# Kernel tuning notes

Measured on AMD Instinct MI355X. Metric: run time of the kernel, lower is better.

Reference implementation:

```python
import jax, jax.numpy as jnp
import numpy as np

N = 512          # number of proposals
C = 1024         # in_channels
FLAT = C * 7 * 7 # 50176, fc1 input dim
D = 1024         # hidden / feat_dim / attention dim
SCALE = 1.0 / np.sqrt(float(D))


def setup_inputs() -> dict:
    key = jax.random.key(0)
    ks = jax.random.split(key, 20)
    w = lambda k, shape: (jax.random.normal(k, shape, jnp.float32) * 0.01)
    inp = {"x": jax.random.normal(ks[0], (N, C, 7, 7), jnp.float32)}
    # SelsaHead fc layers
    inp["fc1_w"] = w(ks[1], (D, FLAT)); inp["fc1_b"] = jnp.zeros((D,), jnp.float32)
    inp["fc2_w"] = w(ks[2], (D, D));    inp["fc2_b"] = jnp.zeros((D,), jnp.float32)
    # attention_1 (semantic_aggregation): fc1, fc2, 1x1 conv (stored as [D,D] matrix)
    inp["a1_fc1_w"] = w(ks[3], (D, D)); inp["a1_fc1_b"] = jnp.zeros((D,), jnp.float32)
    inp["a1_fc2_w"] = w(ks[4], (D, D)); inp["a1_fc2_b"] = jnp.zeros((D,), jnp.float32)
    inp["a1_conv_w"] = w(ks[5], (D, D)); inp["a1_conv_b"] = jnp.zeros((D,), jnp.float32)
    # attention_2
    inp["a2_fc1_w"] = w(ks[6], (D, D)); inp["a2_fc1_b"] = jnp.zeros((D,), jnp.float32)
    inp["a2_fc2_w"] = w(ks[7], (D, D)); inp["a2_fc2_b"] = jnp.zeros((D,), jnp.float32)
    inp["a2_conv_w"] = w(ks[8], (D, D)); inp["a2_conv_b"] = jnp.zeros((D,), jnp.float32)
    return inp


def _semantic_aggregation(x, w1, b1, w2, b2, cw, cb):
    # x: [N, D]. Single-head dense attention over proposals, values = x itself.
    q = x @ w1.T + b1                      # [N, D]
    k = x @ w2.T + b2                      # [N, D]
    p = jax.nn.softmax((q @ k.T) * SCALE, axis=-1)  # [N, N]
    out = p @ x                            # [N, D]  (values are raw x)
    return out @ cw.T + cb                 # 1x1 conv == linear [N, D]


def reference(x, fc1_w, fc1_b, fc2_w, fc2_b,
              a1_fc1_w, a1_fc1_b, a1_fc2_w, a1_fc2_b, a1_conv_w, a1_conv_b,
              a2_fc1_w, a2_fc1_b, a2_fc2_w, a2_fc2_b, a2_conv_w, a2_conv_b):
    out = x.reshape(x.shape[0], -1) @ fc1_w.T + fc1_b        # [N, D]
    r1 = _semantic_aggregation(out, a1_fc1_w, a1_fc1_b, a1_fc2_w, a1_fc2_b,
                               a1_conv_w, a1_conv_b)
    h = jax.nn.relu(out + r1)
    h = h @ fc2_w.T + fc2_b                                  # [N, D]
    r2 = _semantic_aggregation(h, a2_fc1_w, a2_fc1_b, a2_fc2_w, a2_fc2_b,
                               a2_conv_w, a2_conv_b)
    return jax.nn.relu(h + r2 + out)                         # [N, D]
```

## Files before the change

### kernel.cpp

```cpp
#include <hip/hip_runtime.h>
#include <hip/hip_bf16.h>

typedef __attribute__((ext_vector_type(8))) short short8;
typedef __attribute__((ext_vector_type(4))) float f32x4;

#define N_PROP 512
#define DHID   1024
#define KFLAT  50176
#define SM_SCALE 0.03125f

__device__ inline short f2bf(float x) {
  __hip_bfloat16 b = __float2bfloat16(x);
  return __builtin_bit_cast(short, b);
}
__device__ inline float bf2f(unsigned short u) {
  unsigned int x = (unsigned int)u << 16;
  return __builtin_bit_cast(float, x);
}

__global__ __launch_bounds__(1024, 4)
void gemm_fc1(const float* __restrict__ A, const float* __restrict__ B,
              __hip_bfloat16* __restrict__ parts)
{
  constexpr int BK = 32, BKP = 40;
  constexpr int KLEN = 1568, NT = KLEN / BK;
  __shared__ short sA[2][256 * BKP];
  __shared__ short sB[2][256 * BKP];

  const int n = gridDim.x;
  int lid = blockIdx.x;
  lid = (lid & 7) * (n >> 3) + (lid >> 3);
  const int y    = lid >> 3;
  const int tile = lid & 7;
  const int tm = tile >> 2;
  const int tn = tile & 3;

  const int k0 = y * KLEN;

  const int tid  = threadIdx.x;
  const int lane = tid & 63;
  const int wid  = tid >> 6;
  const int wr = wid >> 2, wc = wid & 3;
  const int l16 = lane & 15, kq = lane >> 4;

  const float* Ab = A + (size_t)(tm * 256) * KFLAT;
  const float* Bb = B + (size_t)(tn * 256) * KFLAT;

  const int srow = tid >> 2;
  const int scol = (tid & 3) * 8;

  f32x4 acc[4][4];
  #pragma unroll
  for (int i = 0; i < 4; ++i)
    #pragma unroll
    for (int j = 0; j < 4; ++j)
      acc[i][j] = (f32x4){0.f, 0.f, 0.f, 0.f};

  float4 ra0, ra1, rb0, rb1;

  auto loadAB = [&](int kk) {
    const float* pa = Ab + (size_t)srow * KFLAT + kk + scol;
    const float* pb = Bb + (size_t)srow * KFLAT + kk + scol;
    ra0 = *(const float4*)pa; ra1 = *(const float4*)(pa + 4);
    rb0 = *(const float4*)pb; rb1 = *(const float4*)(pb + 4);
  };
  auto storeAB = [&](int b) {
    short8 s;
    s[0]=f2bf(ra0.x); s[1]=f2bf(ra0.y); s[2]=f2bf(ra0.z); s[3]=f2bf(ra0.w);
    s[4]=f2bf(ra1.x); s[5]=f2bf(ra1.y); s[6]=f2bf(ra1.z); s[7]=f2bf(ra1.w);
    *(short8*)&sA[b][srow * BKP + scol] = s;
    s[0]=f2bf(rb0.x); s[1]=f2bf(rb0.y); s[2]=f2bf(rb0.z); s[3]=f2bf(rb0.w);
    s[4]=f2bf(rb1.x); s[5]=f2bf(rb1.y); s[6]=f2bf(rb1.z); s[7]=f2bf(rb1.w);
    *(short8*)&sB[b][srow * BKP + scol] = s;
  };
  auto compute = [&](int b) {
    short8 af[4], bf[4];
    #pragma unroll
    for (int i = 0; i < 4; ++i)
      af[i] = *(short8*)&sA[b][(wr * 64 + i * 16 + l16) * BKP + kq * 8];
    #pragma unroll
    for (int j = 0; j < 4; ++j)
      bf[j] = *(short8*)&sB[b][(wc * 64 + j * 16 + l16) * BKP + kq * 8];
    #pragma unroll
    for (int i = 0; i < 4; ++i)
      #pragma unroll
      for (int j = 0; j < 4; ++j)
        acc[i][j] = __builtin_amdgcn_mfma_f32_16x16x32_bf16(af[i], bf[j], acc[i][j], 0, 0, 0);
  };

  loadAB(k0);
  storeAB(0);
  loadAB(k0 + BK);
  __syncthreads();

  int cur = 0;
  for (int t = 0; t < NT; ++t) {
    if (t + 1 < NT) {
      storeAB(cur ^ 1);
      if (t + 2 < NT) loadAB(k0 + (t + 2) * BK);
    }
    compute(cur);
    __syncthreads();
    cur ^= 1;
  }

  __hip_bfloat16* P = parts + (size_t)y * (N_PROP * DHID);
  const int crow0 = tm * 256 + wr * 64;
  const int ccol0 = tn * 256 + wc * 64;
  #pragma unroll
  for (int i = 0; i < 4; ++i)
    #pragma unroll
    for (int j = 0; j < 4; ++j)
      #pragma unroll
      for (int e = 0; e < 4; ++e) {
        int r = crow0 + i * 16 + kq * 4 + e;
        int c = ccol0 + j * 16 + l16;
        P[(size_t)r * DHID + c] = __float2bfloat16(acc[i][j][e]);
      }
}

template<int BM, int BN, int BK, int MINW>
__global__ __launch_bounds__(256, MINW)
void gemm_nt(const float* __restrict__ A, int lda,
             const float* __restrict__ B1, const float* __restrict__ B2, int ldb,
             float* __restrict__ C, __hip_bfloat16* __restrict__ Cb, int ldc,
             int tiles_per_slice, int tiles_n,
             int klen, int ktot,
             size_t c_split_stride, size_t c_z_stride,
             const float* __restrict__ bias1, const float* __restrict__ bias2,
             const float* __restrict__ res1, const float* __restrict__ res2,
             float* __restrict__ Ct, int ldct,
             int do_relu)
{
  constexpr int BKP = BK + 8;
  constexpr int WM = BM / 2, WN = BN / 2;
  constexpr int FM = WM / 16, FN = WN / 16;
  constexpr int NCH = BK / 8;
  constexpr int CHA = (BM * BK) / (8 * 256);
  constexpr int CHB = (BN * BK) / (8 * 256);

  __shared__ short As[BM * BKP];
  __shared__ short Bs[BN * BKP];

  const int n = gridDim.x;
  int lid = blockIdx.x;
  lid = (lid & 7) * (n >> 3) + (lid >> 3);

  const int y    = lid / tiles_per_slice;
  const int tile = lid % tiles_per_slice;
  const int tm = tile / tiles_n;
  const int tn = tile % tiles_n;

  const int k0 = y * klen;
  const int krem = ktot - k0;
  const int klen_eff = krem < klen ? krem : klen;
  const int nt = klen_eff / BK;

  const size_t coff = (size_t)y * c_split_stride + (size_t)blockIdx.z * c_z_stride;
  if (C)  C  += coff;
  if (Cb) Cb += coff;
  const float* B    = blockIdx.z ? B2 : B1;
  const float* bias = blockIdx.z ? bias2 : bias1;

  const int tid  = threadIdx.x;
  const int lane = tid & 63;
  const int wid  = tid >> 6;
  const int wm = wid >> 1, wn = wid & 1;
  const int l16 = lane & 15, kq = lane >> 4;

  const float* Abase = A + (size_t)(tm * BM) * lda;
  const float* Bbase = B + (size_t)(tn * BN) * ldb;

  f32x4 acc[FM][FN];
  #pragma unroll
  for (int i = 0; i < FM; ++i)
    #pragma unroll
    for (int j = 0; j < FN; ++j)
      acc[i][j] = (f32x4){0.f, 0.f, 0.f, 0.f};

  float4 ra[CHA][2], rb[CHB][2];

  auto loadA = [&](int kk) {
    #pragma unroll
    for (int i = 0; i < CHA; ++i) {
      int ch = tid + i * 256;
      int r = ch / NCH, cc = ch % NCH;
      const float* p = Abase + (size_t)r * lda + kk + cc * 8;
      ra[i][0] = *(const float4*)p;
      ra[i][1] = *(const float4*)(p + 4);
    }
  };
  auto loadB = [&](int kk) {
    #pragma unroll
    for (int i = 0; i < CHB; ++i) {
      int ch = tid + i * 256;
      int r = ch / NCH, cc = ch % NCH;
      const float* p = Bbase + (size_t)r * ldb + kk + cc * 8;
      rb[i][0] = *(const float4*)p;
      rb[i][1] = *(const float4*)(p + 4);
    }
  };
  auto storeAB = [&]() {
    #pragma unroll
    for (int i = 0; i < CHA; ++i) {
      int ch = tid + i * 256;
      int r = ch / NCH, cc = ch % NCH;
      float4 u = ra[i][0], v = ra[i][1];
      short8 s;
      s[0]=f2bf(u.x); s[1]=f2bf(u.y); s[2]=f2bf(u.z); s[3]=f2bf(u.w);
      s[4]=f2bf(v.x); s[5]=f2bf(v.y); s[6]=f2bf(v.z); s[7]=f2bf(v.w);
      *(short8*)&As[r * BKP + cc * 8] = s;
    }
    #pragma unroll
    for (int i = 0; i < CHB; ++i) {
      int ch = tid + i * 256;
      int r = ch / NCH, cc = ch % NCH;
      float4 u = rb[i][0], v = rb[i][1];
      short8 s;
      s[0]=f2bf(u.x); s[1]=f2bf(u.y); s[2]=f2bf(u.z); s[3]=f2bf(u.w);
      s[4]=f2bf(v.x); s[5]=f2bf(v.y); s[6]=f2bf(v.z); s[7]=f2bf(v.w);
      *(short8*)&Bs[r * BKP + cc * 8] = s;
    }
  };

  loadA(k0); loadB(k0);
  storeAB();
  __syncthreads();

  for (int t = 0; t < nt; ++t) {
    if (t + 1 < nt) { loadA(k0 + (t + 1) * BK); loadB(k0 + (t + 1) * BK); }

    #pragma unroll
    for (int ks = 0; ks < BK / 32; ++ks) {
      short8 af[FM], bf[FN];
      #pragma unroll
      for (int i = 0; i < FM; ++i)
        af[i] = *(short8*)&As[(wm * WM + i * 16 + l16) * BKP + ks * 32 + kq * 8];
      #pragma unroll
      for (int j = 0; j < FN; ++j)
        bf[j] = *(short8*)&Bs[(wn * WN + j * 16 + l16) * BKP + ks * 32 + kq * 8];
      #pragma unroll
      for (int i = 0; i < FM; ++i)
        #pragma unroll
        for (int j = 0; j < FN; ++j)
          acc[i][j] = __builtin_amdgcn_mfma_f32_16x16x32_bf16(af[i], bf[j], acc[i][j], 0, 0, 0);
    }

    __syncthreads();
    if (t + 1 < nt) storeAB();
    __syncthreads();
  }

  const int crow0 = tm * BM + wm * WM;
  const int ccol0 = tn * BN + wn * WN;
  #pragma unroll
  for (int i = 0; i < FM; ++i)
    #pragma unroll
    for (int j = 0; j < FN; ++j)
      #pragma unroll
      for (int e = 0; e < 4; ++e) {
        int r = crow0 + i * 16 + kq * 4 + e;
        int c = ccol0 + j * 16 + l16;
        float v = acc[i][j][e];
        if (bias) v += bias[c];
        if (res1) v += res1[(size_t)r * ldc + c];
        if (res2) v += res2[(size_t)r * ldc + c];
        if (do_relu) v = fmaxf(v, 0.f);
        if (Cb) Cb[(size_t)r * ldc + c] = __float2bfloat16(v);
        else    C [(size_t)r * ldc + c] = v;
        if (Ct) Ct[(size_t)c * ldct + r] = v;
      }
}

__global__ __launch_bounds__(256)
void reduce_bias(const __hip_bfloat16* __restrict__ parts, int sk, size_t stride,
                 const float* __restrict__ bias, float* __restrict__ out)
{
  int idx4 = blockIdx.x * 256 + threadIdx.x;
  int c4 = idx4 & (DHID / 4 - 1);
  float4 b = *(const float4*)(bias + (size_t)c4 * 4);
  float s0 = b.x, s1 = b.y, s2 = b.z, s3 = b.w;
  for (int i = 0; i < sk; ++i) {
    const __hip_bfloat16* p = parts + (size_t)i * stride + (size_t)idx4 * 4;
    ushort4 u = *(const ushort4*)p;
    s0 += bf2f(u.x); s1 += bf2f(u.y); s2 += bf2f(u.z); s3 += bf2f(u.w);
  }
  float4 o = {s0, s1, s2, s3};
  *(float4*)(out + (size_t)idx4 * 4) = o;
}

__global__ __launch_bounds__(256)
void transpose_k(const float* __restrict__ in, float* __restrict__ out, int R, int Cc)
{
  __shared__ float t[32][33];
  int bx = blockIdx.x * 32;
  int by = blockIdx.y * 32;
  int tx = threadIdx.x & 31, ty = threadIdx.x >> 5;
  #pragma unroll
  for (int i = 0; i < 4; ++i)
    t[ty + i * 8][tx] = in[(size_t)(by + ty + i * 8) * Cc + bx + tx];
  __syncthreads();
  #pragma unroll
  for (int i = 0; i < 4; ++i)
    out[(size_t)(bx + ty + i * 8) * R + by + tx] = t[tx][ty + i * 8];
}

__global__ __launch_bounds__(256)
void softmax_rows(float* __restrict__ x, float scale)
{
  int row = blockIdx.x;
  float* p = x + (size_t)row * N_PROP;
  int tid = threadIdx.x;
  float a = p[tid] * scale;
  float b = p[tid + 256] * scale;
  float m = fmaxf(a, b);
  #pragma unroll
  for (int o = 32; o > 0; o >>= 1) m = fmaxf(m, __shfl_xor(m, o));
  __shared__ float sm[4], ss[4];
  int w = tid >> 6;
  if ((tid & 63) == 0) sm[w] = m;
  __syncthreads();
  m = fmaxf(fmaxf(sm[0], sm[1]), fmaxf(sm[2], sm[3]));
  float ea = __expf(a - m), eb = __expf(b - m);
  float s = ea + eb;
  #pragma unroll
  for (int o = 32; o > 0; o >>= 1) s += __shfl_xor(s, o);
  if ((tid & 63) == 0) ss[w] = s;
  __syncthreads();
  s = ss[0] + ss[1] + ss[2] + ss[3];
  float inv = 1.f / s;
  p[tid] = ea * inv;
  p[tid + 256] = eb * inv;
}

extern "C" void kernel_launch(void* const* d_in, const int* in_sizes, int n_in,
                              void* d_out, int out_size, void* d_ws, size_t ws_size,
                              hipStream_t stream)
{
  (void)in_sizes; (void)n_in; (void)out_size; (void)ws_size;
  const float* x      = (const float*)d_in[0];
  const float* fc1_w  = (const float*)d_in[1];
  const float* fc1_b  = (const float*)d_in[2];
  const float* fc2_w  = (const float*)d_in[3];
  const float* fc2_b  = (const float*)d_in[4];
  const float* a1w1   = (const float*)d_in[5];
  const float* a1b1   = (const float*)d_in[6];
  const float* a1w2   = (const float*)d_in[7];
  const float* a1b2   = (const float*)d_in[8];
  const float* a1cw   = (const float*)d_in[9];
  const float* a1cb   = (const float*)d_in[10];
  const float* a2w1   = (const float*)d_in[11];
  const float* a2b1   = (const float*)d_in[12];
  const float* a2w2   = (const float*)d_in[13];
  const float* a2b2   = (const float*)d_in[14];
  const float* a2cw   = (const float*)d_in[15];
  const float* a2cb   = (const float*)d_in[16];
  float* out = (float*)d_out;

  char* ws = (char*)d_ws;
  const size_t SZ = (size_t)N_PROP * DHID * 4;
  float* out0   = (float*)(ws + 0 * SZ);
  float* h0     = (float*)(ws + 1 * SZ);
  float* h1     = (float*)(ws + 2 * SZ);
  float* T      = (float*)(ws + 3 * SZ);
  float* q      = (float*)(ws + 4 * SZ);
  float* k      = (float*)(ws + 5 * SZ);
  float* att    = (float*)(ws + 6 * SZ);
  float* logits = (float*)(ws + 7 * SZ);
  __hip_bfloat16* parts =
      (__hip_bfloat16*)(ws + 7 * SZ + (size_t)N_PROP * N_PROP * 4);

  const size_t ND = (size_t)N_PROP * DHID;
  const int SK = 32;
  dim3 blk(256);

  gemm_fc1<<<dim3(8 * SK), dim3(1024), 0, stream>>>(x, fc1_w, parts);
  reduce_bias<<<(N_PROP * DHID) / 1024, blk, 0, stream>>>(parts, SK, ND, fc1_b, out0);

  transpose_k<<<dim3(DHID / 32, N_PROP / 32), blk, 0, stream>>>(out0, T, N_PROP, DHID);
  gemm_nt<32, 64, 128, 2><<<dim3(256, 1, 2), blk, 0, stream>>>(
      out0, DHID, a1w1, a1w2, DHID,
      q, nullptr, DHID,
      256, 16, DHID, DHID,
      0, ND,
      a1b1, a1b2, nullptr, nullptr, nullptr, 0, 0);
  gemm_nt<32, 32, 128, 2><<<dim3(256), blk, 0, stream>>>(
      q, DHID, k, nullptr, DHID,
      logits, nullptr, N_PROP,
      256, 16, DHID, DHID,
      0, 0,
      nullptr, nullptr, nullptr, nullptr, nullptr, 0, 0);
  softmax_rows<<<N_PROP, blk, 0, stream>>>(logits, SM_SCALE);
  gemm_nt<32, 64, 128, 2><<<dim3(256), blk, 0, stream>>>(
      logits, N_PROP, T, nullptr, N_PROP,
      att, nullptr, DHID,
      256, 16, N_PROP, N_PROP,
      0, 0,
      nullptr, nullptr, nullptr, nullptr, nullptr, 0, 0);
  gemm_nt<32, 64, 128, 2><<<dim3(256), blk, 0, stream>>>(
      att, DHID, a1cw, nullptr, DHID,
      h0, nullptr, DHID,
      256, 16, DHID, DHID,
      0, 0,
      a1cb, nullptr, out0, nullptr, nullptr, 0, 1);
  gemm_nt<32, 64, 128, 2><<<dim3(256), blk, 0, stream>>>(
      h0, DHID, fc2_w, nullptr, DHID,
      h1, nullptr, DHID,
      256, 16, DHID, DHID,
      0, 0,
      fc2_b, nullptr, nullptr, nullptr, T, N_PROP, 0);

  gemm_nt<32, 64, 128, 2><<<dim3(256, 1, 2), blk, 0, stream>>>(
      h1, DHID, a2w1, a2w2, DHID,
      q, nullptr, DHID,
      256, 16, DHID, DHID,
      0, ND,
      a2b1, a2b2, nullptr, nullptr, nullptr, 0, 0);
  gemm_nt<32, 32, 128, 2><<<dim3(256), blk, 0, stream>>>(
      q, DHID, k, nullptr, DHID,
      logits, nullptr, N_PROP,
      256, 16, DHID, DHID,
      0, 0,
      nullptr, nullptr, nullptr, nullptr, nullptr, 0, 0);
  softmax_rows<<<N_PROP, blk, 0, stream>>>(logits, SM_SCALE);
  gemm_nt<32, 64, 128, 2><<<dim3(256), blk, 0, stream>>>(
      logits, N_PROP, T, nullptr, N_PROP,
      att, nullptr, DHID,
      256, 16, N_PROP, N_PROP,
      0, 0,
      nullptr, nullptr, nullptr, nullptr, nullptr, 0, 0);
  gemm_nt<32, 64, 128, 2><<<dim3(256), blk, 0, stream>>>(
      att, DHID, a2cw, nullptr, DHID,
      out, nullptr, DHID,
      256, 16, DHID, DHID,
      0, 0,
      a2cb, nullptr, h1, out0, nullptr, 0, 1);
}
```

Before: 218.0 us.

## Swizzle fc1 LDS tiles with XOR layout and use lightweight LDS-only barriers

Replaces the padded LDS rows (stride 40) in the fc1 GEMM with an unpadded 32-element row and an XOR swizzle of the 8-element chunk index, to avoid bank conflicts while shrinking LDS use. It also replaces __syncthreads with a barrier that waits only on LDS counters, so outstanding global prefetch loads are not drained at each barrier. The swizzled layout must match between writes and reads, and the weaker barrier relies on global loads not being needed before the sync.

```diff
diff --git a/kernel.cpp b/kernel.cpp
--- a/kernel.cpp
+++ b/kernel.cpp
@@ -18,14 +18,20 @@
   return __builtin_bit_cast(float, x);
 }
 
+__device__ inline void pinned_bar() {
+  asm volatile("s_waitcnt lgkmcnt(0)" ::: "memory");
+  __builtin_amdgcn_s_barrier();
+  asm volatile("" ::: "memory");
+}
+
 __global__ __launch_bounds__(1024, 4)
 void gemm_fc1(const float* __restrict__ A, const float* __restrict__ B,
               __hip_bfloat16* __restrict__ parts)
 {
-  constexpr int BK = 32, BKP = 40;
+  constexpr int BK = 32;
   constexpr int KLEN = 1568, NT = KLEN / BK;
-  __shared__ short sA[2][256 * BKP];
-  __shared__ short sB[2][256 * BKP];
+  __shared__ short sA[2][256 * 32];
+  __shared__ short sB[2][256 * 32];
 
   const int n = gridDim.x;
   int lid = blockIdx.x;
@@ -47,7 +53,8 @@
   const float* Bb = B + (size_t)(tn * 256) * KFLAT;
 
   const int srow = tid >> 2;
-  const int scol = (tid & 3) * 8;
+  const int sc   = tid & 3;
+  const int sphys = sc ^ ((srow >> 1) & 3);
 
   f32x4 acc[4][4];
   #pragma unroll
@@ -59,8 +66,8 @@
   float4 ra0, ra1, rb0, rb1;
 
   auto loadAB = [&](int kk) {
-    const float* pa = Ab + (size_t)srow * KFLAT + kk + scol;
-    const float* pb = Bb + (size_t)srow * KFLAT + kk + scol;
+    const float* pa = Ab + (size_t)srow * KFLAT + kk + sc * 8;
+    const float* pb = Bb + (size_t)srow * KFLAT + kk + sc * 8;
     ra0 = *(const float4*)pa; ra1 = *(const float4*)(pa + 4);
     rb0 = *(const float4*)pb; rb1 = *(const float4*)(pb + 4);
   };
@@ -68,19 +75,25 @@
     short8 s;
     s[0]=f2bf(ra0.x); s[1]=f2bf(ra0.y); s[2]=f2bf(ra0.z); s[3]=f2bf(ra0.w);
     s[4]=f2bf(ra1.x); s[5]=f2bf(ra1.y); s[6]=f2bf(ra1.z); s[7]=f2bf(ra1.w);
-    *(short8*)&sA[b][srow * BKP + scol] = s;
+    *(short8*)&sA[b][srow * 32 + sphys * 8] = s;
     s[0]=f2bf(rb0.x); s[1]=f2bf(rb0.y); s[2]=f2bf(rb0.z); s[3]=f2bf(rb0.w);
     s[4]=f2bf(rb1.x); s[5]=f2bf(rb1.y); s[6]=f2bf(rb1.z); s[7]=f2bf(rb1.w);
-    *(short8*)&sB[b][srow * BKP + scol] = s;
+    *(short8*)&sB[b][srow * 32 + sphys * 8] = s;
   };
   auto compute = [&](int b) {
     short8 af[4], bf[4];
     #pragma unroll
-    for (int i = 0; i < 4; ++i)
-      af[i] = *(short8*)&sA[b][(wr * 64 + i * 16 + l16) * BKP + kq * 8];
-    #pragma unroll
-    for (int j = 0; j < 4; ++j)
-      bf[j] = *(short8*)&sB[b][(wc * 64 + j * 16 + l16) * BKP + kq * 8];
+    for (int i = 0; i < 4; ++i) {
+      int R  = wr * 64 + i * 16 + l16;
+      int ph = kq ^ ((R >> 1) & 3);
+      af[i] = *(short8*)&sA[b][R * 32 + ph * 8];
+    }
+    #pragma unroll
+    for (int j = 0; j < 4; ++j) {
+      int R  = wc * 64 + j * 16 + l16;
+      int ph = kq ^ ((R >> 1) & 3);
+      bf[j] = *(short8*)&sB[b][R * 32 + ph * 8];
+    }
     #pragma unroll
     for (int i = 0; i < 4; ++i)
       #pragma unroll
@@ -91,7 +104,7 @@
   loadAB(k0);
   storeAB(0);
   loadAB(k0 + BK);
-  __syncthreads();
+  pinned_bar();
 
   int cur = 0;
   for (int t = 0; t < NT; ++t) {
@@ -100,7 +113,7 @@
       if (t + 2 < NT) loadAB(k0 + (t + 2) * BK);
     }
     compute(cur);
-    __syncthreads();
+    pinned_bar();
     cur ^= 1;
   }
 
@@ -225,7 +238,7 @@
 
   loadA(k0); loadB(k0);
   storeAB();
-  __syncthreads();
+  pinned_bar();
 
   for (int t = 0; t < nt; ++t) {
     if (t + 1 < nt) { loadA(k0 + (t + 1) * BK); loadB(k0 + (t + 1) * BK); }
@@ -246,9 +259,9 @@
           acc[i][j] = __builtin_amdgcn_mfma_f32_16x16x32_bf16(af[i], bf[j], acc[i][j], 0, 0, 0);
     }
 
-    __syncthreads();
+    pinned_bar();
     if (t + 1 < nt) storeAB();
-    __syncthreads();
+    pinned_bar();
   }
 
   const int crow0 = tm * BM + wm * WM;
```

New measurement: 221.1 us. No clear change (+1.4%).
